# Kernel optimization log

Measured on AMD Instinct MI355X. Metric: run time of the kernel, lower is better.

## Reference

```python
import jax, jax.numpy as jnp
import numpy as np

B, T, I, U = 64, 1024, 512, 1024


def ternary_quantize(w):
    # alpha = mean|w|; threshold = 0.7*alpha; map to {-alpha, 0, alpha}
    alpha = jnp.mean(jnp.abs(w))
    thr = 0.7 * alpha
    w_t = jnp.where(jnp.abs(w) < thr, jnp.zeros_like(w), jnp.sign(w))
    return alpha * w_t


def setup_inputs() -> dict:
    key = jax.random.key(0)
    k1, k2, k3 = jax.random.split(key, 3)
    x = jax.random.normal(k1, (B, T, I), dtype=jnp.float32)
    kernel = jax.random.normal(k2, (I, 4 * U), dtype=jnp.float32) * 0.05
    recurrent_kernel = jax.random.normal(k3, (U, 4 * U), dtype=jnp.float32) * 0.05
    # keras unit_forget_bias: zeros except ones on the forget-gate quarter
    bias = jnp.concatenate([jnp.zeros((U,)), jnp.ones((U,)), jnp.zeros((2 * U,))]).astype(jnp.float32)
    return {"x": x, "kernel": kernel, "recurrent_kernel": recurrent_kernel, "bias": bias}


def reference(x, kernel, recurrent_kernel, bias):
    kq = ternary_quantize(kernel)            # [I, 4U]
    rq = ternary_quantize(recurrent_kernel)  # [U, 4U]
    # Precompute input projection for all timesteps (math identical to per-step matmul)
    xz = jnp.einsum('bti,ig->btg', x, kq) + bias  # [B, T, 4U]
    xz_t = jnp.transpose(xz, (1, 0, 2))           # [T, B, 4U]

    def step(carry, zx):
        h, c = carry
        z = zx + h @ rq                            # [B, 4U]
        zi, zf, zg, zo = jnp.split(z, 4, axis=-1)  # keras gate order i, f, c, o
        i = jax.nn.sigmoid(zi)
        f = jax.nn.sigmoid(zf)
        g = jnp.tanh(zg)
        o = jax.nn.sigmoid(zo)
        c_new = f * c + i * g
        h_new = o * jnp.tanh(c_new)
        return (h_new, c_new), h_new

    h0 = jnp.zeros((x.shape[0], U), dtype=x.dtype)
    c0 = jnp.zeros((x.shape[0], U), dtype=x.dtype)
    _, hs = jax.lax.scan(step, (h0, c0), xz_t)     # hs: [T, B, U]
    return jnp.transpose(hs, (1, 0, 2))            # return_sequences=True -> [B, T, U]
```

## Files before the change

kernel.cpp:

```cpp
#include <hip/hip_runtime.h>
#include <hip/hip_bf16.h>


typedef __attribute__((ext_vector_type(8))) __bf16 bf16x8;
typedef __attribute__((ext_vector_type(4))) float f32x4;

#define NWG 256
#define WGT 512
#define T_N 1024

__global__ void absum_kernel(const float* __restrict__ w, int n,
                             double* __restrict__ partial) {
  __shared__ double sd[256];
  double s = 0.0;
  for (int i = blockIdx.x * 256 + threadIdx.x; i < n; i += 256 * 256)
    s += fabs((double)w[i]);
  sd[threadIdx.x] = s;
  __syncthreads();
  for (int k = 128; k > 0; k >>= 1) {
    if (threadIdx.x < k) sd[threadIdx.x] += sd[threadIdx.x + k];
    __syncthreads();
  }
  if (threadIdx.x == 0) partial[blockIdx.x] = sd[0];
}

__global__ void alpha_finalize(const double* __restrict__ pk,
                               const double* __restrict__ pr,
                               float* __restrict__ alphas) {
  __shared__ double sd[256];
  int t = threadIdx.x;
  sd[t] = pk[t];
  __syncthreads();
  for (int s = 128; s > 0; s >>= 1) {
    if (t < s) sd[t] += sd[t + s];
    __syncthreads();
  }
  if (t == 0) alphas[0] = (float)(sd[0] / (512.0 * 4096.0));
  __syncthreads();
  sd[t] = pr[t];
  __syncthreads();
  for (int s = 128; s > 0; s >>= 1) {
    if (t < s) sd[t] += sd[t + s];
    __syncthreads();
  }
  if (t == 0) alphas[1] = (float)(sd[0] / (1024.0 * 4096.0));
}

__global__ void quant_kernel(const float* __restrict__ w, int kbits,
                             const float* __restrict__ alphas, int ai,
                             __hip_bfloat16* __restrict__ wt, int total) {
  int idx = blockIdx.x * 256 + threadIdx.x;
  if (idx >= total) return;
  float thr = 0.7f * alphas[ai];
  int K = 1 << kbits;
  int c = idx >> kbits;
  int k = idx & (K - 1);
  float v = w[k * 4096 + (c & 3) * 1024 + (c >> 2)];
  float q = (fabsf(v) < thr) ? 0.0f : ((v > 0.0f) ? 1.0f : ((v < 0.0f) ? -1.0f : 0.0f));
  wt[idx] = __float2bfloat16(q);
}

__device__ __forceinline__ bf16x8 cvt2(f32x4 a, f32x4 b) {
  bf16x8 r;
  r[0] = (__bf16)a[0]; r[1] = (__bf16)a[1];
  r[2] = (__bf16)a[2]; r[3] = (__bf16)a[3];
  r[4] = (__bf16)b[0]; r[5] = (__bf16)b[1];
  r[6] = (__bf16)b[2]; r[7] = (__bf16)b[3];
  return r;
}
__device__ __forceinline__ void ld16cc(bf16x8* d, const __hip_bfloat16* p) {
  asm volatile("global_load_dwordx4 %0, %1, off sc0 sc1"
               : "=v"(*d) : "v"(p) : "memory");
}
__device__ __forceinline__ void st_cc2(__hip_bfloat16* p, unsigned bits) {
  asm volatile("global_store_short %0, %1, off sc0 sc1" ::"v"(p), "v"(bits)
               : "memory");
}
__device__ __forceinline__ void stflag(int* p, int v) {
  asm volatile("global_store_dword %0, %1, off sc0 sc1" ::"v"(p), "v"(v)
               : "memory");
}
__device__ __forceinline__ int ldflag(const int* p) {
  int v;
  asm volatile("global_load_dword %0, %1, off sc0 sc1\n\ts_waitcnt vmcnt(0)"
               : "=v"(v) : "v"(p) : "memory");
  return v;
}
__device__ __forceinline__ unsigned bf16b(float f) {
  return (unsigned)__builtin_bit_cast(unsigned short, __float2bfloat16(f));
}
__device__ __forceinline__ float sigm(float z) { return 1.0f / (1.0f + __expf(-z)); }
__device__ __forceinline__ float tanhx(float z) {
  float e = __expf(-2.0f * fabsf(z));
  return __builtin_copysignf((1.0f - e) / (1.0f + e), z);
}

__global__ void __launch_bounds__(WGT, 2)
lstm_persist(const float* __restrict__ bias4, const float* __restrict__ alphas,
             const float* __restrict__ x,
             const __hip_bfloat16* __restrict__ wtk,
             const __hip_bfloat16* __restrict__ wtr,
             __hip_bfloat16* __restrict__ hbuf,
             float* __restrict__ out,
             int* __restrict__ flags) {
  extern __shared__ char lds[];
  char* lwtk = lds;
  float* lz = (float*)(lds + 131072);
  float* lxz = (float*)(lds + 147968);
  int* lmeta = (int*)(lds + 156416);

  const int tid = threadIdx.x;
  const int wg = blockIdx.x;
  const int lane = tid & 63;
  const int wave = tid >> 6;
  const int r16 = lane & 15;
  const int kb8 = (lane >> 4) << 3;

  const int g = wg >> 5;
  const int u = wg & 31;
  const int rb0 = g << 3;

  if (tid < 4) lmeta[tid] = 0;

  int* myflag = flags + ((g << 2) + (u >> 3)) * 32 + (u & 7);
  const int* pollp = flags + ((g << 2) + (wave & 3)) * 32 + (lane & 7);

  for (int it = tid; it < 8192; it += WGT) {
    int c = it >> 6, kk = (it & 63) << 3;
    bf16x8 v = *(const bf16x8*)(wtk + (size_t)(u * 128 + c) * 512 + kk);
    *(bf16x8*)(lwtk + (c << 10) + ((kk << 1) ^ ((c & 7) << 4))) = v;
  }

  const int ks0 = (wave & 3) << 8;
  bf16x8 bw[8][4];
  {
    const __hip_bfloat16* wb =
        wtr + (size_t)(u * 128 + ((wave >> 2) << 6) + r16) * 1024 + ks0 + kb8;
#pragma unroll
    for (int ks = 0; ks < 8; ++ks)
#pragma unroll
      for (int nt = 0; nt < 4; ++nt)
        bw[ks][nt] = *(const bf16x8*)(wb + (size_t)nt * 16 * 1024 + (ks << 5));
  }

  const float ak = alphas[0];
  const float ar = alphas[1];

  const int rl = tid >> 5;
  const int ul = tid & 31;
  float bias_c[4];
#pragma unroll
  for (int gg = 0; gg < 4; ++gg)
    bias_c[gg] = bias4[gg * 1024 + u * 32 + ul];
  float cst = 0.0f;
  __hip_bfloat16* hst = hbuf + (g << 13) + (rl << 10) + u * 32 + ul;
  float* outp = out + ((size_t)(rb0 + rl) << 20) + u * 32 + ul;

  auto xproj = [&](int tt, int par) {
    const float* xr =
        x + ((size_t)(rb0 + (r16 & 7)) << 19) + ((size_t)tt << 9) + kb8;
    const int cloc = (wave << 4) + r16;
    const char* bbase = lwtk + (cloc << 10);
    const int bxor = (cloc & 7) << 4;
    f32x4 a = {0.f, 0.f, 0.f, 0.f};
#pragma unroll
    for (int kw = 0; kw < 16; ++kw) {
      bf16x8 af = cvt2(*(const f32x4*)(xr + kw * 32),
                       *(const f32x4*)(xr + kw * 32 + 4));
      bf16x8 bf = *(const bf16x8*)(bbase + ((((kw << 5) + kb8) << 1) ^ bxor));
      a = __builtin_amdgcn_mfma_f32_16x16x32_bf16(af, bf, a, 0, 0, 0);
    }
    if (lane < 32) {
      float* dst = lxz + par * 1056 + (wave << 4) + (lane & 15);
#pragma unroll
      for (int j = 0; j < 4; ++j)
        dst[(((lane >> 4) << 2) + j) * 132] = a[j];
    }
  };

  __syncthreads();
  xproj(0, 0);

  for (int t = 0; t < T_N; ++t) {
    {
      f32x4 acc[4];
#pragma unroll
      for (int nt = 0; nt < 4; ++nt) acc[nt] = (f32x4){0.f, 0.f, 0.f, 0.f};
      if (t > 0) {
        if (wave < 4) {
          for (;;) {
            int v = (lane < 8) ? ldflag(pollp) : 0x7fffffff;
            if (__all(v >= t)) break;
          }
          if (lane == 0)
            __hip_atomic_store(&lmeta[wave], t, __ATOMIC_RELEASE,
                               __HIP_MEMORY_SCOPE_WORKGROUP);
        } else {
          while (__hip_atomic_load(&lmeta[wave - 4], __ATOMIC_ACQUIRE,
                                   __HIP_MEMORY_SCOPE_WORKGROUP) < t) {}
        }
        bf16x8 fr[8];
        if (r16 < 8) {
          const __hip_bfloat16* hrow =
              hbuf + ((t & 1) << 16) + (g << 13) + (r16 << 10) + ks0 + kb8;
#pragma unroll
          for (int ks = 0; ks < 8; ++ks) ld16cc(&fr[ks], hrow + (ks << 5));
        } else {
#pragma unroll
          for (int ks = 0; ks < 8; ++ks)
#pragma unroll
            for (int j = 0; j < 8; ++j) fr[ks][j] = (__bf16)0.0f;
        }
        asm volatile("s_waitcnt vmcnt(0)" ::: "memory");
        __builtin_amdgcn_sched_barrier(0);
#pragma unroll
        for (int ks = 0; ks < 8; ++ks)
#pragma unroll
          for (int nt = 0; nt < 4; ++nt)
            acc[nt] = __builtin_amdgcn_mfma_f32_16x16x32_bf16(
                fr[ks], bw[ks][nt], acc[nt], 0, 0, 0);
      }
      if (lane < 32) {
        float* dst = lz + (wave & 3) * 1056 + ((wave >> 2) << 6) + (lane & 15);
#pragma unroll
        for (int nt = 0; nt < 4; ++nt)
#pragma unroll
          for (int j = 0; j < 4; ++j)
            dst[(((lane >> 4) << 2) + j) * 132 + (nt << 4)] = acc[nt][j];
      }
    }
    __syncthreads();

    float ho = 0.0f;
    if (tid < 256) {
      f32x4 z0 = *(const f32x4*)(lz + 0 * 1056 + rl * 132 + (ul << 2));
      f32x4 z1 = *(const f32x4*)(lz + 1 * 1056 + rl * 132 + (ul << 2));
      f32x4 z2 = *(const f32x4*)(lz + 2 * 1056 + rl * 132 + (ul << 2));
      f32x4 z3 = *(const f32x4*)(lz + 3 * 1056 + rl * 132 + (ul << 2));
      f32x4 z = z0 + z1 + z2 + z3;
      f32x4 xv = *(const f32x4*)(lxz + (t & 1) * 1056 + rl * 132 + (ul << 2));
      float zi = ak * xv[0] + bias_c[0] + ar * z[0];
      float zf = ak * xv[1] + bias_c[1] + ar * z[1];
      float zg = ak * xv[2] + bias_c[2] + ar * z[2];
      float zo = ak * xv[3] + bias_c[3] + ar * z[3];
      float ig = sigm(zi), fg = sigm(zf), gg = tanhx(zg), og = sigm(zo);
      float cn = fg * cst + ig * gg;
      cst = cn;
      ho = og * tanhx(cn);
      st_cc2(hst + (((t + 1) & 1) << 16), bf16b(ho));
      asm volatile("s_waitcnt vmcnt(0)" ::: "memory");
    }
    __syncthreads();

    if (wave == 4 && lane == 0) stflag(myflag, t + 1);

    if (tid < 256) outp[(size_t)t << 10] = ho;
    if (t != T_N - 1) xproj(t + 1, (t + 1) & 1);
  }
}

extern "C" void kernel_launch(void* const* d_in, const int* in_sizes, int n_in,
                              void* d_out, int out_size, void* d_ws, size_t ws_size,
                              hipStream_t stream) {
  const float* x = (const float*)d_in[0];
  const float* wk = (const float*)d_in[1];
  const float* wr = (const float*)d_in[2];
  const float* bs = (const float*)d_in[3];
  float* out = (float*)d_out;
  char* ws = (char*)d_ws;

  float* alphas = (float*)(ws + 0);
  double* pk = (double*)(ws + 1024);
  int* flags = (int*)(ws + 4096);
  double* pr = (double*)(ws + 8192);
  __hip_bfloat16* wtk = (__hip_bfloat16*)(ws + 16384);
  __hip_bfloat16* wtr = (__hip_bfloat16*)(ws + 16384 + (4 << 20));
  __hip_bfloat16* hbuf = (__hip_bfloat16*)(ws + 16384 + (12 << 20));

  absum_kernel<<<256, 256, 0, stream>>>(wk, 512 * 4096, pk);
  absum_kernel<<<256, 256, 0, stream>>>(wr, 1024 * 4096, pr);
  alpha_finalize<<<1, 256, 0, stream>>>(pk, pr, alphas);
  quant_kernel<<<(4096 * 512) / 256, 256, 0, stream>>>(wk, 9, alphas, 0, wtk,
                                                       4096 * 512);
  quant_kernel<<<(4096 * 1024) / 256, 256, 0, stream>>>(wr, 10, alphas, 1, wtr,
                                                        4096 * 1024);
  (void)hipMemsetAsync(flags, 0, 4096);

  const int smem = 131072 + 16896 + 8448 + 64;
  (void)hipFuncSetAttribute((const void*)lstm_persist,
                            hipFuncAttributeMaxDynamicSharedMemorySize, smem);
  void* args[] = {(void*)&bs,  (void*)&alphas, (void*)&x,   (void*)&wtk,
                  (void*)&wtr, (void*)&hbuf,   (void*)&out, (void*)&flags};
  (void)hipLaunchCooperativeKernel((void*)lstm_persist, dim3(NWG), dim3(WGT),
                                   args, smem, stream);
}
```

Baseline: 11.14 ms.

## Embed step tag in hidden-state values to replace separate flag synchronization

Each workgroup now writes its hidden state as fp32 with a step-dependent offset added, so consumers can tell data is fresh by checking the values themselves rather than polling separate flags. This drops the flag store after the barrier, the LDS relay between waves, and one fence round-trip per timestep. All waves poll and reload the h data directly, subtracting the offset before the bf16 conversion. The cost is twice the bytes per h load (fp32 instead of bf16), more polling traffic, and a staleness check that relies on |h|<1 and the tag spacing, which also slightly perturbs precision.

Result: slower. 11.94 ms (+7.1%).

```diff
diff --git a/kernel.cpp b/kernel.cpp
--- a/kernel.cpp
+++ b/kernel.cpp
@@ -68,26 +68,19 @@
   r[6] = (__bf16)b[2]; r[7] = (__bf16)b[3];
   return r;
 }
-__device__ __forceinline__ void ld16cc(bf16x8* d, const __hip_bfloat16* p) {
+__device__ __forceinline__ void ldf4cc(f32x4* d, const float* p) {
   asm volatile("global_load_dwordx4 %0, %1, off sc0 sc1"
                : "=v"(*d) : "v"(p) : "memory");
 }
-__device__ __forceinline__ void st_cc2(__hip_bfloat16* p, unsigned bits) {
-  asm volatile("global_store_short %0, %1, off sc0 sc1" ::"v"(p), "v"(bits)
-               : "memory");
-}
-__device__ __forceinline__ void stflag(int* p, int v) {
-  asm volatile("global_store_dword %0, %1, off sc0 sc1" ::"v"(p), "v"(v)
-               : "memory");
-}
-__device__ __forceinline__ int ldflag(const int* p) {
-  int v;
+__device__ __forceinline__ float ldfcc(const float* p) {
+  float v;
   asm volatile("global_load_dword %0, %1, off sc0 sc1\n\ts_waitcnt vmcnt(0)"
                : "=v"(v) : "v"(p) : "memory");
   return v;
 }
-__device__ __forceinline__ unsigned bf16b(float f) {
-  return (unsigned)__builtin_bit_cast(unsigned short, __float2bfloat16(f));
+__device__ __forceinline__ void stfcc(float* p, float v) {
+  asm volatile("global_store_dword %0, %1, off sc0 sc1" ::"v"(p), "v"(v)
+               : "memory");
 }
 __device__ __forceinline__ float sigm(float z) { return 1.0f / (1.0f + __expf(-z)); }
 __device__ __forceinline__ float tanhx(float z) {
@@ -100,14 +93,12 @@
              const float* __restrict__ x,
              const __hip_bfloat16* __restrict__ wtk,
              const __hip_bfloat16* __restrict__ wtr,
-             __hip_bfloat16* __restrict__ hbuf,
-             float* __restrict__ out,
-             int* __restrict__ flags) {
+             float* __restrict__ henc,
+             float* __restrict__ out) {
   extern __shared__ char lds[];
   char* lwtk = lds;
   float* lz = (float*)(lds + 131072);
   float* lxz = (float*)(lds + 147968);
-  int* lmeta = (int*)(lds + 156416);
 
   const int tid = threadIdx.x;
   const int wg = blockIdx.x;
@@ -120,11 +111,6 @@
   const int u = wg & 31;
   const int rb0 = g << 3;
 
-  if (tid < 4) lmeta[tid] = 0;
-
-  int* myflag = flags + ((g << 2) + (u >> 3)) * 32 + (u & 7);
-  const int* pollp = flags + ((g << 2) + (wave & 3)) * 32 + (lane & 7);
-
   for (int it = tid; it < 8192; it += WGT) {
     int c = it >> 6, kk = (it & 63) << 3;
     bf16x8 v = *(const bf16x8*)(wtk + (size_t)(u * 128 + c) * 512 + kk);
@@ -153,8 +139,11 @@
   for (int gg = 0; gg < 4; ++gg)
     bias_c[gg] = bias4[gg * 1024 + u * 32 + ul];
   float cst = 0.0f;
-  __hip_bfloat16* hst = hbuf + (g << 13) + (rl << 10) + u * 32 + ul;
+  float* hstf = henc + (((g << 3) + rl) << 10) + u * 32 + ul;
   float* outp = out + ((size_t)(rb0 + rl) << 20) + u * 32 + ul;
+
+  const float* hldb = henc + ((((g << 3) + (r16 & 7)) << 10)) + ks0 + kb8;
+  const float* canp = henc + (((g << 3) + 7) << 10) + ks0 + ((lane & 7) << 5) + 31;
 
   auto xproj = [&](int tt, int par) {
     const float* xr =
@@ -187,31 +176,52 @@
 #pragma unroll
       for (int nt = 0; nt < 4; ++nt) acc[nt] = (f32x4){0.f, 0.f, 0.f, 0.f};
       if (t > 0) {
-        if (wave < 4) {
+        const float cexp = (float)(4 * ((t - 1) & 3) + 2);
+        const int poff = (t & 1) << 16;
+        {
+          const float* cp = canp + poff;
           for (;;) {
-            int v = (lane < 8) ? ldflag(pollp) : 0x7fffffff;
-            if (__all(v >= t)) break;
+            float v = (lane < 8) ? ldfcc(cp) : cexp;
+            if (__all(fabsf(v - cexp) < 1.002f)) break;
+            __builtin_amdgcn_s_sleep(1);
           }
-          if (lane == 0)
-            __hip_atomic_store(&lmeta[wave], t, __ATOMIC_RELEASE,
-                               __HIP_MEMORY_SCOPE_WORKGROUP);
-        } else {
-          while (__hip_atomic_load(&lmeta[wave - 4], __ATOMIC_ACQUIRE,
-                                   __HIP_MEMORY_SCOPE_WORKGROUP) < t) {}
         }
         bf16x8 fr[8];
-        if (r16 < 8) {
-          const __hip_bfloat16* hrow =
-              hbuf + ((t & 1) << 16) + (g << 13) + (r16 << 10) + ks0 + kb8;
-#pragma unroll
-          for (int ks = 0; ks < 8; ++ks) ld16cc(&fr[ks], hrow + (ks << 5));
-        } else {
-#pragma unroll
-          for (int ks = 0; ks < 8; ++ks)
-#pragma unroll
-            for (int j = 0; j < 8; ++j) fr[ks][j] = (__bf16)0.0f;
+#pragma unroll
+        for (int ks = 0; ks < 8; ++ks)
+#pragma unroll
+          for (int j = 0; j < 8; ++j) fr[ks][j] = (__bf16)0.0f;
+        const float* hb = hldb + poff;
+        const f32x4 c4 = {cexp, cexp, cexp, cexp};
+#pragma unroll
+        for (int half = 0; half < 2; ++half) {
+          f32x4 e[8];
+          for (;;) {
+            if (r16 < 8) {
+#pragma unroll
+              for (int ks = 0; ks < 4; ++ks) {
+                ldf4cc(&e[2 * ks], hb + (((half << 2) + ks) << 5));
+                ldf4cc(&e[2 * ks + 1], hb + (((half << 2) + ks) << 5) + 4);
+              }
+              asm volatile("s_waitcnt vmcnt(0)" ::: "memory");
+            }
+            float dev = 0.0f;
+            if (r16 < 8) {
+#pragma unroll
+              for (int i = 0; i < 8; ++i)
+#pragma unroll
+                for (int j = 0; j < 4; ++j)
+                  dev = fmaxf(dev, fabsf(e[i][j] - cexp));
+            }
+            if (__all(dev < 1.002f)) break;
+            __builtin_amdgcn_s_sleep(1);
+          }
+          if (r16 < 8) {
+#pragma unroll
+            for (int ks = 0; ks < 4; ++ks)
+              fr[(half << 2) + ks] = cvt2(e[2 * ks] - c4, e[2 * ks + 1] - c4);
+          }
         }
-        asm volatile("s_waitcnt vmcnt(0)" ::: "memory");
         __builtin_amdgcn_sched_barrier(0);
 #pragma unroll
         for (int ks = 0; ks < 8; ++ks)
@@ -231,7 +241,6 @@
     }
     __syncthreads();
 
-    float ho = 0.0f;
     if (tid < 256) {
       f32x4 z0 = *(const f32x4*)(lz + 0 * 1056 + rl * 132 + (ul << 2));
       f32x4 z1 = *(const f32x4*)(lz + 1 * 1056 + rl * 132 + (ul << 2));
@@ -246,15 +255,13 @@
       float ig = sigm(zi), fg = sigm(zf), gg = tanhx(zg), og = sigm(zo);
       float cn = fg * cst + ig * gg;
       cst = cn;
-      ho = og * tanhx(cn);
-      st_cc2(hst + (((t + 1) & 1) << 16), bf16b(ho));
-      asm volatile("s_waitcnt vmcnt(0)" ::: "memory");
+      float ho = og * tanhx(cn);
+      float cw = (float)(4 * (t & 3) + 2);
+      stfcc(hstf + (((t + 1) & 1) << 16), cw + ho);
+      outp[(size_t)t << 10] = ho;
     }
     __syncthreads();
 
-    if (wave == 4 && lane == 0) stflag(myflag, t + 1);
-
-    if (tid < 256) outp[(size_t)t << 10] = ho;
     if (t != T_N - 1) xproj(t + 1, (t + 1) & 1);
   }
 }
@@ -271,11 +278,10 @@
 
   float* alphas = (float*)(ws + 0);
   double* pk = (double*)(ws + 1024);
-  int* flags = (int*)(ws + 4096);
   double* pr = (double*)(ws + 8192);
   __hip_bfloat16* wtk = (__hip_bfloat16*)(ws + 16384);
   __hip_bfloat16* wtr = (__hip_bfloat16*)(ws + 16384 + (4 << 20));
-  __hip_bfloat16* hbuf = (__hip_bfloat16*)(ws + 16384 + (12 << 20));
+  float* henc = (float*)(ws + 16384 + (12 << 20));
 
   absum_kernel<<<256, 256, 0, stream>>>(wk, 512 * 4096, pk);
   absum_kernel<<<256, 256, 0, stream>>>(wr, 1024 * 4096, pr);
@@ -284,13 +290,13 @@
                                                        4096 * 512);
   quant_kernel<<<(4096 * 1024) / 256, 256, 0, stream>>>(wr, 10, alphas, 1, wtr,
                                                         4096 * 1024);
-  (void)hipMemsetAsync(flags, 0, 4096);
-
-  const int smem = 131072 + 16896 + 8448 + 64;
+  (void)hipMemsetAsync(henc, 0, 2 * 8 * 8 * 1024 * 4);
+
+  const int smem = 131072 + 16896 + 8448;
   (void)hipFuncSetAttribute((const void*)lstm_persist,
                             hipFuncAttributeMaxDynamicSharedMemorySize, smem);
-  void* args[] = {(void*)&bs,  (void*)&alphas, (void*)&x,   (void*)&wtk,
-                  (void*)&wtr, (void*)&hbuf,   (void*)&out, (void*)&flags};
+  void* args[] = {(void*)&bs,  (void*)&alphas, (void*)&x, (void*)&wtk,
+                  (void*)&wtr, (void*)&henc,   (void*)&out};
   (void)hipLaunchCooperativeKernel((void*)lstm_persist, dim3(NWG), dim3(WGT),
                                    args, smem, stream);
 }
```
